# Performance work log

Measured on AMD Instinct MI355X. Metric: run time of the kernel, lower is better.

Reference implementation:

```python
import jax, jax.numpy as jnp
import numpy as np

N, L, H, Q = 64, 258, 1024, 256
WINDOW = 16.0
DEV_POW = 128.0  # 2 * (window/2)^2, Luong local-p sigma = D/2


def setup_inputs() -> dict:
    key = jax.random.key(0)
    k1, k2, k3, k4, k5, k6 = jax.random.split(key, 6)
    encoder_outputs = jax.random.normal(k1, (N, L, H), dtype=jnp.float32)
    decoder_h_t = jax.random.normal(k2, (N, Q, H), dtype=jnp.float32)
    src_len = jax.random.randint(k3, (N,), 32, L + 1).astype(jnp.int32)
    # window centers within each source sentence
    p_t = jax.random.uniform(k4, (N,), dtype=jnp.float32) * (src_len.astype(jnp.float32) - 1.0)
    W_a = jax.random.normal(k5, (H, H), dtype=jnp.float32) * (1.0 / np.sqrt(H))
    W_c = jax.random.normal(k6, (H, 2 * H), dtype=jnp.float32) * (1.0 / np.sqrt(2 * H))
    return {"encoder_outputs": encoder_outputs, "decoder_h_t": decoder_h_t,
            "src_len": src_len, "p_t": p_t, "W_a": W_a, "W_c": W_c}


def reference(encoder_outputs, decoder_h_t, src_len, p_t, W_a, W_c):
    n, l, h = encoder_outputs.shape
    idx = jnp.arange(l, dtype=jnp.float32)  # index_matrix, length == max_length == L

    # local_p window: [p_t - D, p_t + D], clamped to [0, src_len]
    src_end = src_len.astype(jnp.float32)
    attn_start = jnp.maximum(p_t - WINDOW, 0.0)          # [N]
    attn_end = jnp.minimum(p_t + WINDOW, src_end)        # [N]
    mask = (idx[None, :] < attn_start[:, None]) | (idx[None, :] > attn_end[:, None])  # [N,L]

    # Luong 'general' score: h_t^T W_a h_s -> [N,Q,L]
    score = jnp.einsum('nqh,hk,nlk->nql', decoder_h_t, W_a, encoder_outputs)

    score = jnp.where(mask[:, None, :], -1e9, score)
    align = jax.nn.softmax(score, axis=2)                 # [N,Q,L]

    # gaussian reweighting centered at p_t
    gauss = jnp.exp(-((idx[None, :] - p_t[:, None]) ** 2) / DEV_POW)  # [N,L]
    align = align * gauss[:, None, :]

    context = jnp.einsum('nql,nlh->nqh', align, encoder_outputs)      # [N,Q,H]
    cat = jnp.concatenate([context, decoder_h_t], axis=2)             # [N,Q,2H]
    return jnp.tanh(cat @ W_c.T)                                      # [N,Q,H]
```

## Files before the change

kernel.cpp:

```cpp
#include <hip/hip_runtime.h>
#include <hip/hip_bf16.h>
#include <cstdint>

#define DEVINL __device__ __forceinline__

typedef __attribute__((ext_vector_type(8))) short short8;
typedef __attribute__((ext_vector_type(4))) float f32x4;
typedef __attribute__((ext_vector_type(4))) unsigned short u16x4;

static constexpr int NB = 64, LL = 258, HH = 1024, QQ = 256;
static constexpr int WROWS = 33;
static constexpr int MU = 2176;
static constexpr int VTN = 4096;

static constexpr size_t OFF_META = 0;
static constexpr size_t SZ_WE   = (size_t)MU * HH * 2;
static constexpr size_t OFF_WEHI = 1024;
static constexpr size_t OFF_WELO = OFF_WEHI + SZ_WE;
static constexpr size_t OFF_WAHI = OFF_WELO + SZ_WE;
static constexpr size_t OFF_WALO = OFF_WAHI + (size_t)HH * HH * 2;
static constexpr size_t OFF_WCBF = OFF_WALO + (size_t)HH * HH * 2;
static constexpr size_t OFF_HBF  = OFF_WCBF + (size_t)HH * 2 * HH * 2;
static constexpr size_t OFF_U    = OFF_HBF + (size_t)NB * QQ * HH * 2;
static constexpr size_t OFF_UHI  = OFF_U;
static constexpr size_t OFF_ULO  = OFF_U + (size_t)MU * HH * 2;
static constexpr size_t OFF_CTX  = OFF_U + (size_t)MU * HH * 4;
static constexpr size_t OFF_VT   = OFF_CTX + (size_t)NB * QQ * HH * 2;

DEVINL unsigned short f2bf(float x) {
    union { float f; uint32_t u; } v; v.f = x;
    uint32_t u = v.u;
    uint32_t r = (u + 0x7FFFu + ((u >> 16) & 1u)) >> 16;
    return (unsigned short)r;
}
DEVINL float bf2f(unsigned short b) {
    union { uint32_t u; float f; } v; v.u = ((uint32_t)b) << 16;
    return v.f;
}

template <typename T>
DEVINL void lds_load16(const T* g, T* l) {
    __builtin_amdgcn_global_load_lds(
        (const __attribute__((address_space(1))) void*)g,
        (__attribute__((address_space(3))) void*)l, 16, 0, 0);
}

DEVINL float fast_tanh(float x) {
    float e = __expf(2.0f * x);
    return 1.0f - 2.0f / (e + 1.0f);
}

DEVINL void window_of(float p, int sl, int& ls, int& lc) {
    float se = (float)sl;
    float s = fmaxf(p - 16.0f, 0.0f);
    float e = fminf(p + 16.0f, se);
    ls = (int)ceilf(s);
    int le = (int)floorf(e); if (le > LL - 1) le = LL - 1;
    lc = le - ls + 1;
    if (lc < 0) lc = 0;
    if (lc > WROWS) lc = WROWS;
}

__global__ __launch_bounds__(256) void k_prep(const float* __restrict__ enc,
                                              const float* __restrict__ ht,
                                              const float* __restrict__ pt,
                                              const int* __restrict__ slen,
                                              const float* __restrict__ Wa,
                                              const float* __restrict__ Wc,
                                              unsigned short* __restrict__ wehi,
                                              unsigned short* __restrict__ welo,
                                              unsigned short* __restrict__ wahi,
                                              unsigned short* __restrict__ walo,
                                              unsigned short* __restrict__ wcbf,
                                              unsigned short* __restrict__ hbf) {
    const int b = blockIdx.x, t = threadIdx.x;
    if (b < MU) {
        int r = b;
        const float* src = nullptr;
        bool valid = false;
        if (r < NB * WROWS) {
            int n = r / WROWS, li = r - n * WROWS;
            int ls, lc;
            window_of(pt[n], slen[n], ls, lc);
            if (li < lc) { valid = true; src = enc + ((size_t)n * LL + ls + li) * HH; }
        }
        f32x4 v;
        if (valid) v = ((const f32x4*)src)[t];
        else { v[0] = 0.f; v[1] = 0.f; v[2] = 0.f; v[3] = 0.f; }
        u16x4 h, l;
#pragma unroll
        for (int j = 0; j < 4; ++j) {
            unsigned short hb = f2bf(v[j]);
            h[j] = hb;
            l[j] = f2bf(v[j] - bf2f(hb));
        }
        size_t o = (size_t)r * HH / 4 + t;
        ((u16x4*)wehi)[o] = h;
        ((u16x4*)welo)[o] = l;
    } else if (b < MU + 1024) {
        int i = (b - MU) * 256 + t;
        f32x4 v = ((const f32x4*)Wa)[i];
        u16x4 h, l;
#pragma unroll
        for (int j = 0; j < 4; ++j) {
            unsigned short hb = f2bf(v[j]);
            h[j] = hb;
            l[j] = f2bf(v[j] - bf2f(hb));
        }
        ((u16x4*)wahi)[i] = h;
        ((u16x4*)walo)[i] = l;
    } else if (b < MU + 1024 + 2048) {
        int i = (b - MU - 1024) * 256 + t;
        f32x4 v = ((const f32x4*)Wc)[i];
        u16x4 h;
#pragma unroll
        for (int j = 0; j < 4; ++j) h[j] = f2bf(v[j]);
        ((u16x4*)wcbf)[i] = h;
    } else {
        int i = (b - MU - 3072) * 256 + t;
        f32x4 v = ((const f32x4*)ht)[i];
        u16x4 h;
#pragma unroll
        for (int j = 0; j < 4; ++j) h[j] = f2bf(v[j]);
        ((u16x4*)hbf)[i] = h;
    }
}

__global__ __launch_bounds__(256) void k_wgemm(const unsigned short* __restrict__ wehi,
                                               const unsigned short* __restrict__ welo,
                                               const unsigned short* __restrict__ wahi,
                                               const unsigned short* __restrict__ walo,
                                               const unsigned short* __restrict__ wcbf,
                                               unsigned short* __restrict__ Uhi,
                                               unsigned short* __restrict__ Ulo,
                                               unsigned short* __restrict__ VT) {
    __shared__ unsigned short smem[24576];
    const int tid = threadIdx.x;
    const int w = tid >> 6, lane = tid & 63;
    const int wr = w >> 1, wc = w & 1;
    const int r16 = lane & 15, khalf = lane >> 4, rg = lane >> 4;
    const int srow = tid >> 2;
    const int scol = ((tid & 3) ^ ((tid >> 3) & 3)) * 8;
    const int kslot = (khalf ^ ((r16 >> 1) & 3)) * 8;
    const int bid = blockIdx.x;

    if (bid < 272) {
        const int m0 = (bid >> 3) * 64;
        const int n0 = (bid & 7) * 128;
        f32x4 acc[2][4] = {};

        auto stage = [&](int buf, int kb) {
            lds_load16(wehi + (size_t)(m0 + srow) * HH + kb + scol, &smem[buf * 2048 + tid * 8]);
            lds_load16(welo + (size_t)(m0 + srow) * HH + kb + scol, &smem[4096 + buf * 2048 + tid * 8]);
#pragma unroll
            for (int i = 0; i < 2; ++i) {
                lds_load16(wahi + (size_t)(n0 + i * 64 + srow) * HH + kb + scol,
                           &smem[8192 + buf * 4096 + i * 2048 + tid * 8]);
                lds_load16(walo + (size_t)(n0 + i * 64 + srow) * HH + kb + scol,
                           &smem[16384 + buf * 4096 + i * 2048 + tid * 8]);
            }
        };

        stage(0, 0);
        for (int t = 0; t < 32; ++t) {
            const int buf = t & 1;
            asm volatile("s_waitcnt vmcnt(0)" ::: "memory");
            __builtin_amdgcn_s_barrier();
            short8 ah[2], al[2], bh[4], bl[4];
#pragma unroll
            for (int f = 0; f < 2; ++f) {
                int ai = buf * 2048 + (wr * 32 + f * 16 + r16) * 32 + kslot;
                ah[f] = *(const short8*)&smem[ai];
                al[f] = *(const short8*)&smem[4096 + ai];
            }
#pragma unroll
            for (int nf = 0; nf < 4; ++nf) {
                int bi = buf * 4096 + (wc * 64 + nf * 16 + r16) * 32 + kslot;
                bh[nf] = *(const short8*)&smem[8192 + bi];
                bl[nf] = *(const short8*)&smem[16384 + bi];
            }
            if (t + 1 < 32) stage(buf ^ 1, (t + 1) * 32);
            asm volatile("s_waitcnt lgkmcnt(0)" ::: "memory");
            __builtin_amdgcn_sched_barrier(0);
#pragma unroll
            for (int mf = 0; mf < 2; ++mf)
#pragma unroll
                for (int nf = 0; nf < 4; ++nf) {
                    acc[mf][nf] = __builtin_amdgcn_mfma_f32_16x16x32_bf16(ah[mf], bh[nf], acc[mf][nf], 0, 0, 0);
                    acc[mf][nf] = __builtin_amdgcn_mfma_f32_16x16x32_bf16(ah[mf], bl[nf], acc[mf][nf], 0, 0, 0);
                    acc[mf][nf] = __builtin_amdgcn_mfma_f32_16x16x32_bf16(al[mf], bh[nf], acc[mf][nf], 0, 0, 0);
                }
            __builtin_amdgcn_s_barrier();
        }
#pragma unroll
        for (int mf = 0; mf < 2; ++mf)
#pragma unroll
            for (int nf = 0; nf < 4; ++nf)
#pragma unroll
                for (int r = 0; r < 4; ++r) {
                    int m = m0 + wr * 32 + mf * 16 + rg * 4 + r;
                    int nn = n0 + wc * 64 + nf * 16 + r16;
                    float v = acc[mf][nf][r];
                    unsigned short h = f2bf(v);
                    Uhi[(size_t)m * HH + nn] = h;
                    Ulo[(size_t)m * HH + nn] = f2bf(v - bf2f(h));
                }
    } else {
        const int b2 = bid - 272;
        const int m0 = (b2 / 17) * 64;
        const int n0 = (b2 % 17) * 128;
        f32x4 acc[2][4] = {};

        auto stage = [&](int buf, int kb) {
            lds_load16(wcbf + (size_t)(m0 + srow) * (2 * HH) + kb + scol, &smem[buf * 2048 + tid * 8]);
#pragma unroll
            for (int i = 0; i < 2; ++i) {
                lds_load16(wehi + (size_t)(n0 + i * 64 + srow) * HH + kb + scol,
                           &smem[8192 + buf * 4096 + i * 2048 + tid * 8]);
                lds_load16(welo + (size_t)(n0 + i * 64 + srow) * HH + kb + scol,
                           &smem[16384 + buf * 4096 + i * 2048 + tid * 8]);
            }
        };

        stage(0, 0);
        for (int t = 0; t < 32; ++t) {
            const int buf = t & 1;
            asm volatile("s_waitcnt vmcnt(0)" ::: "memory");
            __builtin_amdgcn_s_barrier();
            short8 af[2], bh[4], bl[4];
#pragma unroll
            for (int f = 0; f < 2; ++f)
                af[f] = *(const short8*)&smem[buf * 2048 + (wr * 32 + f * 16 + r16) * 32 + kslot];
#pragma unroll
            for (int nf = 0; nf < 4; ++nf) {
                int bi = buf * 4096 + (wc * 64 + nf * 16 + r16) * 32 + kslot;
                bh[nf] = *(const short8*)&smem[8192 + bi];
                bl[nf] = *(const short8*)&smem[16384 + bi];
            }
            if (t + 1 < 32) stage(buf ^ 1, (t + 1) * 32);
            asm volatile("s_waitcnt lgkmcnt(0)" ::: "memory");
            __builtin_amdgcn_sched_barrier(0);
#pragma unroll
            for (int mf = 0; mf < 2; ++mf)
#pragma unroll
                for (int nf = 0; nf < 4; ++nf) {
                    acc[mf][nf] = __builtin_amdgcn_mfma_f32_16x16x32_bf16(af[mf], bh[nf], acc[mf][nf], 0, 0, 0);
                    acc[mf][nf] = __builtin_amdgcn_mfma_f32_16x16x32_bf16(af[mf], bl[nf], acc[mf][nf], 0, 0, 0);
                }
            __builtin_amdgcn_s_barrier();
        }
#pragma unroll
        for (int mf = 0; mf < 2; ++mf)
#pragma unroll
            for (int nf = 0; nf < 4; ++nf)
#pragma unroll
                for (int r = 0; r < 4; ++r) {
                    int o = m0 + wr * 32 + mf * 16 + rg * 4 + r;
                    int wrow = n0 + wc * 64 + nf * 16 + r16;
                    int n = wrow / WROWS, li = wrow - n * WROWS;
                    if (n < NB)
                        VT[(size_t)o * VTN + n * 64 + li] = f2bf(acc[mf][nf][r]);
                }
    }
}

__global__ __launch_bounds__(256) void k_attn2(const float* __restrict__ ht,
                                               const unsigned short* __restrict__ Uhi,
                                               const unsigned short* __restrict__ Ulo,
                                               const unsigned short* __restrict__ VT,
                                               const float* __restrict__ pt,
                                               const int* __restrict__ slen,
                                               unsigned short* __restrict__ ctxP) {
    __shared__ float sPart[4][32 * 48];
    __shared__ float sScore[32 * 48];
    __shared__ unsigned short sPhi[32 * 72];
    __shared__ unsigned short sPlo[32 * 72];

    const int tid = threadIdx.x;
    const int w = tid >> 6, lane = tid & 63;
    const int n = blockIdx.x >> 3, q0 = (blockIdx.x & 7) * 32;
    int ls, lc;
    window_of(pt[n], slen[n], ls, lc);
    const float p = pt[n];
    const int r16 = lane & 15, khalf = lane >> 4, rg = lane >> 4;

    const float* hbase = ht + ((size_t)(n * QQ + q0)) * HH;
    const unsigned short* uhbase = Uhi + (size_t)n * WROWS * HH;
    const unsigned short* ulbase = Ulo + (size_t)n * WROWS * HH;

    f32x4 acc[2][3] = {};
    for (int ks = 0; ks < 8; ++ks) {
        int kcol = w * 256 + ks * 32 + khalf * 8;
        short8 ah[2], al[2];
#pragma unroll
        for (int mf = 0; mf < 2; ++mf) {
            const float* src = hbase + (size_t)(mf * 16 + r16) * HH + kcol;
            f32x4 v0 = *(const f32x4*)src;
            f32x4 v1 = *(const f32x4*)(src + 4);
            float vv[8] = {v0[0], v0[1], v0[2], v0[3], v1[0], v1[1], v1[2], v1[3]};
#pragma unroll
            for (int j = 0; j < 8; ++j) {
                unsigned short hb = f2bf(vv[j]);
                ah[mf][j] = (short)hb;
                al[mf][j] = (short)f2bf(vv[j] - bf2f(hb));
            }
        }
#pragma unroll
        for (int nf = 0; nf < 3; ++nf) {
            size_t uoff = (size_t)(nf * 16 + r16) * HH + kcol;
            short8 bh = *(const short8*)(uhbase + uoff);
            short8 bl = *(const short8*)(ulbase + uoff);
#pragma unroll
            for (int mf = 0; mf < 2; ++mf) {
                acc[mf][nf] = __builtin_amdgcn_mfma_f32_16x16x32_bf16(ah[mf], bh, acc[mf][nf], 0, 0, 0);
                acc[mf][nf] = __builtin_amdgcn_mfma_f32_16x16x32_bf16(ah[mf], bl, acc[mf][nf], 0, 0, 0);
                acc[mf][nf] = __builtin_amdgcn_mfma_f32_16x16x32_bf16(al[mf], bh, acc[mf][nf], 0, 0, 0);
            }
        }
    }
#pragma unroll
    for (int mf = 0; mf < 2; ++mf)
#pragma unroll
        for (int nf = 0; nf < 3; ++nf)
#pragma unroll
            for (int r = 0; r < 4; ++r)
                sPart[w][(mf * 16 + rg * 4 + r) * 48 + nf * 16 + r16] = acc[mf][nf][r];
    __syncthreads();

    {
        int q = tid >> 3, g = tid & 7;
        float sc6[6];
#pragma unroll
        for (int s = 0; s < 6; ++s) {
            int li = g + 8 * s;
            int o = q * 48 + li;
            sc6[s] = sPart[0][o] + sPart[1][o] + sPart[2][o] + sPart[3][o];
        }
        float mx = -1e30f;
#pragma unroll
        for (int s = 0; s < 6; ++s) { int li = g + 8 * s; if (li < lc) mx = fmaxf(mx, sc6[s]); }
        for (int off = 1; off < 8; off <<= 1) mx = fmaxf(mx, __shfl_xor(mx, off, 8));
        float sum = 0.f, ex[6];
#pragma unroll
        for (int s = 0; s < 6; ++s) {
            int li = g + 8 * s;
            float e = (li < lc) ? __expf(sc6[s] - mx) : 0.f;
            ex[s] = e; sum += e;
        }
        for (int off = 1; off < 8; off <<= 1) sum += __shfl_xor(sum, off, 8);
        float inv = 1.0f / sum;
#pragma unroll
        for (int s = 0; s < 6; ++s) {
            int li = g + 8 * s;
            float d = (float)(ls + li) - p;
            float gs = __expf(-(d * d) * (1.0f / 128.0f));
            sScore[q * 48 + li] = ex[s] * inv * gs;
        }
    }
    __syncthreads();

    {
        int row = tid >> 3, c0 = (tid & 7) * 8;
#pragma unroll
        for (int j = 0; j < 8; ++j) {
            int c = c0 + j;
            float pv = (c < 48) ? sScore[row * 48 + c] : 0.f;
            unsigned short hb = f2bf(pv);
            sPhi[row * 72 + c] = hb;
            sPlo[row * 72 + c] = f2bf(pv - bf2f(hb));
        }
    }
    __syncthreads();

    short8 pa[2][2], plq[2][2];
#pragma unroll
    for (int mf = 0; mf < 2; ++mf)
#pragma unroll
        for (int ks = 0; ks < 2; ++ks) {
            pa[mf][ks]  = *(const short8*)&sPhi[(mf * 16 + r16) * 72 + ks * 32 + khalf * 8];
            plq[mf][ks] = *(const short8*)&sPlo[(mf * 16 + r16) * 72 + ks * 32 + khalf * 8];
        }
    const unsigned short* vtb = VT + n * 64 + khalf * 8;
#pragma unroll
    for (int half = 0; half < 2; ++half) {
        f32x4 accB[2][8] = {};
        const int hcol0 = w * 256 + half * 128;
#pragma unroll
        for (int nf = 0; nf < 8; ++nf) {
            const int o = hcol0 + nf * 16 + r16;
#pragma unroll
            for (int ks = 0; ks < 2; ++ks) {
                short8 bfrag = *(const short8*)(vtb + (size_t)o * VTN + ks * 32);
#pragma unroll
                for (int mf = 0; mf < 2; ++mf) {
                    accB[mf][nf] = __builtin_amdgcn_mfma_f32_16x16x32_bf16(pa[mf][ks], bfrag, accB[mf][nf], 0, 0, 0);
                    accB[mf][nf] = __builtin_amdgcn_mfma_f32_16x16x32_bf16(plq[mf][ks], bfrag, accB[mf][nf], 0, 0, 0);
                }
            }
        }
        const int nt = w * 2 + half;
#pragma unroll
        for (int mf = 0; mf < 2; ++mf) {
            const int rb = q0 + mf * 16;
            const int mt = n * 2 + (rb >> 7);
            const int rowbit = (rb >> 6) & 1;
            const int mq = (rb >> 4) & 3;
#pragma unroll
            for (int pp = 0; pp < 4; ++pp) {
                short8 pk;
#pragma unroll
                for (int r = 0; r < 4; ++r) {
                    pk[r]     = (short)f2bf(accB[mf][2 * pp][r]);
                    pk[4 + r] = (short)f2bf(accB[mf][2 * pp + 1][r]);
                }
                const int widc = rowbit * 2 + (pp >> 1);
                const int fid = mq * 2 + (pp & 1);
                size_t off = ((((size_t)(mt * 8 + nt) * 4 + widc) * 8 + fid) * 64 + lane) * 8;
                *(short8*)&ctxP[off] = pk;
            }
        }
    }
}

__global__ __launch_bounds__(256) void k_out_gemm128(
    const unsigned short* __restrict__ Ahf,
    const unsigned short* __restrict__ Bt,
    const unsigned short* __restrict__ Cp,
    float* __restrict__ out) {
    __shared__ unsigned short sA[128 * 64], sB[128 * 64];

    const int tid = threadIdx.x;
    const int wid = tid >> 6, lane = tid & 63;
    const int bid = blockIdx.x;
    const int swz = (bid & 7) * 128 + (bid >> 3);
    const int mt = swz >> 3, nt = swz & 7;
    const int m0 = mt * 128, n0 = nt * 128;
    const int wr = wid >> 1, wc = wid & 1;
    const int r16 = lane & 15, kg = lane >> 4;

    const int srow8 = lane >> 3;
    const int kswz = ((lane & 7) ^ srow8) * 8;

    f32x4 acc[4][4] = {};

    for (int t = 0; t < 16; ++t) {
        const int kb = t * 64;
        if (t > 0) __syncthreads();
#pragma unroll
        for (int i = 0; i < 4; ++i) {
            int row = i * 32 + wid * 8 + srow8;
            lds_load16(Ahf + (size_t)(m0 + row) * HH + kb + kswz,
                       &sA[i * 2048 + wid * 512]);
            lds_load16(Bt + (size_t)(n0 + row) * (2 * HH) + 1024 + kb + kswz,
                       &sB[i * 2048 + wid * 512]);
        }
        asm volatile("s_waitcnt vmcnt(0)" ::: "memory");
        __syncthreads();

        short8 a[4][2];
#pragma unroll
        for (int mq = 0; mq < 4; ++mq)
#pragma unroll
            for (int ks = 0; ks < 2; ++ks)
                a[mq][ks] = *(const short8*)&sA[(wr * 64 + mq * 16 + r16) * 64 +
                                                (((ks * 4 + kg) ^ (r16 & 7)) * 8)];
#pragma unroll
        for (int nq = 0; nq < 4; ++nq) {
            short8 b0 = *(const short8*)&sB[(wc * 64 + nq * 16 + r16) * 64 +
                                            (((0 + kg) ^ (r16 & 7)) * 8)];
            short8 b1 = *(const short8*)&sB[(wc * 64 + nq * 16 + r16) * 64 +
                                            (((4 + kg) ^ (r16 & 7)) * 8)];
#pragma unroll
            for (int mq = 0; mq < 4; ++mq) {
                acc[mq][nq] = __builtin_amdgcn_mfma_f32_16x16x32_bf16(a[mq][0], b0, acc[mq][nq], 0, 0, 0);
                acc[mq][nq] = __builtin_amdgcn_mfma_f32_16x16x32_bf16(a[mq][1], b1, acc[mq][nq], 0, 0, 0);
            }
        }
    }

    const size_t cbase = (((size_t)(mt * 8 + nt) * 4 + wid) * 8) * 512 + (size_t)lane * 8;
    short8 cv[8];
#pragma unroll
    for (int f = 0; f < 8; ++f)
        cv[f] = *(const short8*)&Cp[cbase + (size_t)f * 512];
#pragma unroll
    for (int mq = 0; mq < 4; ++mq)
#pragma unroll
        for (int nq = 0; nq < 4; ++nq) {
            const int f = mq * 2 + (nq >> 1);
            const int part = (nq & 1) * 4;
            int row = m0 + wr * 64 + mq * 16 + kg * 4;
            int col = n0 + wc * 64 + nq * 16 + r16;
#pragma unroll
            for (int r = 0; r < 4; ++r) {
                float cadd = bf2f((unsigned short)cv[f][part + r]);
                out[(size_t)(row + r) * HH + col] = fast_tanh(acc[mq][nq][r] + cadd);
            }
        }
}

extern "C" void kernel_launch(void* const* d_in, const int* in_sizes, int n_in,
                              void* d_out, int out_size, void* d_ws, size_t ws_size,
                              hipStream_t stream) {
    const float* enc  = (const float*)d_in[0];
    const float* ht   = (const float*)d_in[1];
    const int*   slen = (const int*)d_in[2];
    const float* pt   = (const float*)d_in[3];
    const float* Wa   = (const float*)d_in[4];
    const float* Wc   = (const float*)d_in[5];
    float* out = (float*)d_out;

    char* ws = (char*)d_ws;
    unsigned short* wehi = (unsigned short*)(ws + OFF_WEHI);
    unsigned short* welo = (unsigned short*)(ws + OFF_WELO);
    unsigned short* wahi = (unsigned short*)(ws + OFF_WAHI);
    unsigned short* walo = (unsigned short*)(ws + OFF_WALO);
    unsigned short* wcbf = (unsigned short*)(ws + OFF_WCBF);
    unsigned short* hbf  = (unsigned short*)(ws + OFF_HBF);
    unsigned short* uhi  = (unsigned short*)(ws + OFF_UHI);
    unsigned short* ulo  = (unsigned short*)(ws + OFF_ULO);
    unsigned short* ctxP = (unsigned short*)(ws + OFF_CTX);
    unsigned short* vt   = (unsigned short*)(ws + OFF_VT);

    hipLaunchKernelGGL(k_prep, dim3(MU + 1024 + 2048 + 16384), dim3(256), 0, stream,
                       enc, ht, pt, slen, Wa, Wc, wehi, welo, wahi, walo, wcbf, hbf);
    hipLaunchKernelGGL(k_wgemm, dim3(544), dim3(256), 0, stream,
                       wehi, welo, wahi, walo, wcbf, uhi, ulo, vt);
    hipLaunchKernelGGL(k_attn2, dim3(NB * 8), dim3(256), 0, stream,
                       ht, uhi, ulo, vt, pt, slen, ctxP);
    hipLaunchKernelGGL(k_out_gemm128, dim3(1024), dim3(256), 0, stream,
                       hbf, wcbf, ctxP, out);
}
```

Baseline: 153.3 us.

## Fold context projection into output GEMM as extra K-steps over P and VT

The attention kernel no longer multiplies probabilities by the precomputed VT (encoder times W_c context half) and writes a bf16 context-projection tensor. Instead it writes the hi/lo bf16 split of P, and the output GEMM appends two extra K iterations that multiply P against VT. Those iterations accumulate directly into the tanh output, which removes a large intermediate write and read. The h_t bf16 conversion blocks move from the prep kernel into the wgemm launch so they overlap with the GEMM tiles. The output GEMM does slightly more loop work, and the hi/lo P terms now share one bf16 VT with no intermediate rounding.

```diff
diff --git a/kernel.cpp b/kernel.cpp
--- a/kernel.cpp
+++ b/kernel.cpp
@@ -24,8 +24,8 @@
 static constexpr size_t OFF_U    = OFF_HBF + (size_t)NB * QQ * HH * 2;
 static constexpr size_t OFF_UHI  = OFF_U;
 static constexpr size_t OFF_ULO  = OFF_U + (size_t)MU * HH * 2;
-static constexpr size_t OFF_CTX  = OFF_U + (size_t)MU * HH * 4;
-static constexpr size_t OFF_VT   = OFF_CTX + (size_t)NB * QQ * HH * 2;
+static constexpr size_t OFF_PHL  = OFF_U + (size_t)MU * HH * 4;
+static constexpr size_t OFF_VT   = OFF_PHL + (size_t)NB * QQ * 128 * 2;
 
 DEVINL unsigned short f2bf(float x) {
     union { float f; uint32_t u; } v; v.f = x;
@@ -62,7 +62,6 @@
 }
 
 __global__ __launch_bounds__(256) void k_prep(const float* __restrict__ enc,
-                                              const float* __restrict__ ht,
                                               const float* __restrict__ pt,
                                               const int* __restrict__ slen,
                                               const float* __restrict__ Wa,
@@ -71,8 +70,7 @@
                                               unsigned short* __restrict__ welo,
                                               unsigned short* __restrict__ wahi,
                                               unsigned short* __restrict__ walo,
-                                              unsigned short* __restrict__ wcbf,
-                                              unsigned short* __restrict__ hbf) {
+                                              unsigned short* __restrict__ wcbf) {
     const int b = blockIdx.x, t = threadIdx.x;
     if (b < MU) {
         int r = b;
@@ -109,20 +107,13 @@
         }
         ((u16x4*)wahi)[i] = h;
         ((u16x4*)walo)[i] = l;
-    } else if (b < MU + 1024 + 2048) {
+    } else {
         int i = (b - MU - 1024) * 256 + t;
         f32x4 v = ((const f32x4*)Wc)[i];
         u16x4 h;
 #pragma unroll
         for (int j = 0; j < 4; ++j) h[j] = f2bf(v[j]);
         ((u16x4*)wcbf)[i] = h;
-    } else {
-        int i = (b - MU - 3072) * 256 + t;
-        f32x4 v = ((const f32x4*)ht)[i];
-        u16x4 h;
-#pragma unroll
-        for (int j = 0; j < 4; ++j) h[j] = f2bf(v[j]);
-        ((u16x4*)hbf)[i] = h;
     }
 }
 
@@ -131,18 +122,31 @@
                                                const unsigned short* __restrict__ wahi,
                                                const unsigned short* __restrict__ walo,
                                                const unsigned short* __restrict__ wcbf,
+                                               const float* __restrict__ ht,
                                                unsigned short* __restrict__ Uhi,
                                                unsigned short* __restrict__ Ulo,
-                                               unsigned short* __restrict__ VT) {
+                                               unsigned short* __restrict__ VT,
+                                               unsigned short* __restrict__ hbf) {
     __shared__ unsigned short smem[24576];
     const int tid = threadIdx.x;
+    const int bid = blockIdx.x;
+
+    if (bid >= 544) {
+        int i = (bid - 544) * 256 + tid;
+        f32x4 v = ((const f32x4*)ht)[i];
+        u16x4 h;
+#pragma unroll
+        for (int j = 0; j < 4; ++j) h[j] = f2bf(v[j]);
+        ((u16x4*)hbf)[i] = h;
+        return;
+    }
+
     const int w = tid >> 6, lane = tid & 63;
     const int wr = w >> 1, wc = w & 1;
     const int r16 = lane & 15, khalf = lane >> 4, rg = lane >> 4;
     const int srow = tid >> 2;
     const int scol = ((tid & 3) ^ ((tid >> 3) & 3)) * 8;
     const int kslot = (khalf ^ ((r16 >> 1) & 3)) * 8;
-    const int bid = blockIdx.x;
 
     if (bid < 272) {
         const int m0 = (bid >> 3) * 64;
@@ -267,14 +271,11 @@
 __global__ __launch_bounds__(256) void k_attn2(const float* __restrict__ ht,
                                                const unsigned short* __restrict__ Uhi,
                                                const unsigned short* __restrict__ Ulo,
-                                               const unsigned short* __restrict__ VT,
                                                const float* __restrict__ pt,
                                                const int* __restrict__ slen,
-                                               unsigned short* __restrict__ ctxP) {
+                                               unsigned short* __restrict__ Phl) {
     __shared__ float sPart[4][32 * 48];
     __shared__ float sScore[32 * 48];
-    __shared__ unsigned short sPhi[32 * 72];
-    __shared__ unsigned short sPlo[32 * 72];
 
     const int tid = threadIdx.x;
     const int w = tid >> 6, lane = tid & 63;
@@ -361,71 +362,26 @@
 
     {
         int row = tid >> 3, c0 = (tid & 7) * 8;
+        short8 ph, pl;
 #pragma unroll
         for (int j = 0; j < 8; ++j) {
             int c = c0 + j;
             float pv = (c < 48) ? sScore[row * 48 + c] : 0.f;
             unsigned short hb = f2bf(pv);
-            sPhi[row * 72 + c] = hb;
-            sPlo[row * 72 + c] = f2bf(pv - bf2f(hb));
-        }
-    }
-    __syncthreads();
-
-    short8 pa[2][2], plq[2][2];
-#pragma unroll
-    for (int mf = 0; mf < 2; ++mf)
-#pragma unroll
-        for (int ks = 0; ks < 2; ++ks) {
-            pa[mf][ks]  = *(const short8*)&sPhi[(mf * 16 + r16) * 72 + ks * 32 + khalf * 8];
-            plq[mf][ks] = *(const short8*)&sPlo[(mf * 16 + r16) * 72 + ks * 32 + khalf * 8];
-        }
-    const unsigned short* vtb = VT + n * 64 + khalf * 8;
-#pragma unroll
-    for (int half = 0; half < 2; ++half) {
-        f32x4 accB[2][8] = {};
-        const int hcol0 = w * 256 + half * 128;
-#pragma unroll
-        for (int nf = 0; nf < 8; ++nf) {
-            const int o = hcol0 + nf * 16 + r16;
-#pragma unroll
-            for (int ks = 0; ks < 2; ++ks) {
-                short8 bfrag = *(const short8*)(vtb + (size_t)o * VTN + ks * 32);
-#pragma unroll
-                for (int mf = 0; mf < 2; ++mf) {
-                    accB[mf][nf] = __builtin_amdgcn_mfma_f32_16x16x32_bf16(pa[mf][ks], bfrag, accB[mf][nf], 0, 0, 0);
-                    accB[mf][nf] = __builtin_amdgcn_mfma_f32_16x16x32_bf16(plq[mf][ks], bfrag, accB[mf][nf], 0, 0, 0);
-                }
-            }
-        }
-        const int nt = w * 2 + half;
-#pragma unroll
-        for (int mf = 0; mf < 2; ++mf) {
-            const int rb = q0 + mf * 16;
-            const int mt = n * 2 + (rb >> 7);
-            const int rowbit = (rb >> 6) & 1;
-            const int mq = (rb >> 4) & 3;
-#pragma unroll
-            for (int pp = 0; pp < 4; ++pp) {
-                short8 pk;
-#pragma unroll
-                for (int r = 0; r < 4; ++r) {
-                    pk[r]     = (short)f2bf(accB[mf][2 * pp][r]);
-                    pk[4 + r] = (short)f2bf(accB[mf][2 * pp + 1][r]);
-                }
-                const int widc = rowbit * 2 + (pp >> 1);
-                const int fid = mq * 2 + (pp & 1);
-                size_t off = ((((size_t)(mt * 8 + nt) * 4 + widc) * 8 + fid) * 64 + lane) * 8;
-                *(short8*)&ctxP[off] = pk;
-            }
-        }
+            ph[j] = (short)hb;
+            pl[j] = (short)f2bf(pv - bf2f(hb));
+        }
+        size_t base = (size_t)(n * QQ + q0 + row) * 128;
+        *(short8*)&Phl[base + c0] = ph;
+        *(short8*)&Phl[base + 64 + c0] = pl;
     }
 }
 
 __global__ __launch_bounds__(256) void k_out_gemm128(
     const unsigned short* __restrict__ Ahf,
     const unsigned short* __restrict__ Bt,
-    const unsigned short* __restrict__ Cp,
+    const unsigned short* __restrict__ Phl,
+    const unsigned short* __restrict__ VT,
     float* __restrict__ out) {
     __shared__ unsigned short sA[128 * 64], sB[128 * 64];
 
@@ -435,6 +391,7 @@
     const int swz = (bid & 7) * 128 + (bid >> 3);
     const int mt = swz >> 3, nt = swz & 7;
     const int m0 = mt * 128, n0 = nt * 128;
+    const int nb = mt >> 1;
     const int wr = wid >> 1, wc = wid & 1;
     const int r16 = lane & 15, kg = lane >> 4;
 
@@ -443,16 +400,28 @@
 
     f32x4 acc[4][4] = {};
 
-    for (int t = 0; t < 16; ++t) {
-        const int kb = t * 64;
+    for (int t = 0; t < 18; ++t) {
         if (t > 0) __syncthreads();
-#pragma unroll
-        for (int i = 0; i < 4; ++i) {
-            int row = i * 32 + wid * 8 + srow8;
-            lds_load16(Ahf + (size_t)(m0 + row) * HH + kb + kswz,
-                       &sA[i * 2048 + wid * 512]);
-            lds_load16(Bt + (size_t)(n0 + row) * (2 * HH) + 1024 + kb + kswz,
-                       &sB[i * 2048 + wid * 512]);
+        if (t < 16) {
+            const int kb = t * 64;
+#pragma unroll
+            for (int i = 0; i < 4; ++i) {
+                int row = i * 32 + wid * 8 + srow8;
+                lds_load16(Ahf + (size_t)(m0 + row) * HH + kb + kswz,
+                           &sA[i * 2048 + wid * 512]);
+                lds_load16(Bt + (size_t)(n0 + row) * (2 * HH) + 1024 + kb + kswz,
+                           &sB[i * 2048 + wid * 512]);
+            }
+        } else {
+            const int pc = (t - 16) * 64;
+#pragma unroll
+            for (int i = 0; i < 4; ++i) {
+                int row = i * 32 + wid * 8 + srow8;
+                lds_load16(Phl + (size_t)(m0 + row) * 128 + pc + kswz,
+                           &sA[i * 2048 + wid * 512]);
+                lds_load16(VT + (size_t)(n0 + row) * VTN + nb * 64 + kswz,
+                           &sB[i * 2048 + wid * 512]);
+            }
         }
         asm volatile("s_waitcnt vmcnt(0)" ::: "memory");
         __syncthreads();
@@ -478,24 +447,15 @@
         }
     }
 
-    const size_t cbase = (((size_t)(mt * 8 + nt) * 4 + wid) * 8) * 512 + (size_t)lane * 8;
-    short8 cv[8];
-#pragma unroll
-    for (int f = 0; f < 8; ++f)
-        cv[f] = *(const short8*)&Cp[cbase + (size_t)f * 512];
 #pragma unroll
     for (int mq = 0; mq < 4; ++mq)
 #pragma unroll
         for (int nq = 0; nq < 4; ++nq) {
-            const int f = mq * 2 + (nq >> 1);
-            const int part = (nq & 1) * 4;
             int row = m0 + wr * 64 + mq * 16 + kg * 4;
             int col = n0 + wc * 64 + nq * 16 + r16;
 #pragma unroll
-            for (int r = 0; r < 4; ++r) {
-                float cadd = bf2f((unsigned short)cv[f][part + r]);
-                out[(size_t)(row + r) * HH + col] = fast_tanh(acc[mq][nq][r] + cadd);
-            }
+            for (int r = 0; r < 4; ++r)
+                out[(size_t)(row + r) * HH + col] = fast_tanh(acc[mq][nq][r]);
         }
 }
 
@@ -519,15 +479,15 @@
     unsigned short* hbf  = (unsigned short*)(ws + OFF_HBF);
     unsigned short* uhi  = (unsigned short*)(ws + OFF_UHI);
     unsigned short* ulo  = (unsigned short*)(ws + OFF_ULO);
-    unsigned short* ctxP = (unsigned short*)(ws + OFF_CTX);
+    unsigned short* phl  = (unsigned short*)(ws + OFF_PHL);
     unsigned short* vt   = (unsigned short*)(ws + OFF_VT);
 
-    hipLaunchKernelGGL(k_prep, dim3(MU + 1024 + 2048 + 16384), dim3(256), 0, stream,
-                       enc, ht, pt, slen, Wa, Wc, wehi, welo, wahi, walo, wcbf, hbf);
-    hipLaunchKernelGGL(k_wgemm, dim3(544), dim3(256), 0, stream,
-                       wehi, welo, wahi, walo, wcbf, uhi, ulo, vt);
+    hipLaunchKernelGGL(k_prep, dim3(MU + 1024 + 2048), dim3(256), 0, stream,
+                       enc, pt, slen, Wa, Wc, wehi, welo, wahi, walo, wcbf);
+    hipLaunchKernelGGL(k_wgemm, dim3(544 + 16384), dim3(256), 0, stream,
+                       wehi, welo, wahi, walo, wcbf, ht, uhi, ulo, vt, hbf);
     hipLaunchKernelGGL(k_attn2, dim3(NB * 8), dim3(256), 0, stream,
-                       ht, uhi, ulo, vt, pt, slen, ctxP);
+                       ht, uhi, ulo, pt, slen, phl);
     hipLaunchKernelGGL(k_out_gemm128, dim3(1024), dim3(256), 0, stream,
-                       hbf, wcbf, ctxP, out);
-}
+                       hbf, wcbf, phl, vt, out);
+}
```

After: 137.3 us. 10.4% less time.
